# Optimization experiments

Hardware: AMD Instinct MI355X
Metric: run time of the kernel (lower is better)

Reference implementation:

```python
import jax, jax.numpy as jnp
import numpy as np

TEMP = 0.2
M, K, B = 8192, 128, 100


def setup_inputs() -> dict:
    key = jax.random.key(0)
    k1, k2, k3 = jax.random.split(key, 3)
    f = jax.random.normal(k1, (M, K), dtype=jnp.float32)
    features = f / jnp.linalg.norm(f, axis=1, keepdims=True)
    p = jax.random.normal(k2, (B, K), dtype=jnp.float32)
    protos = p / jnp.linalg.norm(p, axis=1, keepdims=True)
    labels = jax.random.randint(k3, (M,), 0, 2 * B, dtype=jnp.int32)
    proto_labels = jnp.arange(B, dtype=jnp.int32)
    return {"features": features, "labels": labels, "protos": protos, "proto_labels": proto_labels}


def reference(features, labels, protos, proto_labels):
    m = features.shape[0]
    dt = features.dtype
    # base = samples whose label appears among prototype labels
    base = (labels[None, :] == proto_labels[:, None]).any(axis=0)  # [M] bool
    novel = ~base
    nf = novel.astype(dt)
    bf = base.astype(dt)

    S = jnp.matmul(features, features.T) / TEMP          # [M, M] sample-sample logits
    P = jnp.matmul(features, protos.T) / TEMP            # [M, B] sample-proto logits

    # novel-novel pair mask: both novel, off-diagonal (fill_diagonal_(0))
    pair = nf[:, None] * nf[None, :] * (1.0 - jnp.eye(m, dtype=dt))  # [M, M]
    expS = jnp.exp(S)

    # --- novel loss (note: original adds RAW ni_pk.sum, not exp -- faithful) ---
    exp_sum = (expS * pair).sum(axis=1)                  # sum_{j novel, j!=i} exp(S_ij)
    denom = exp_sum + P.sum(axis=1)                      # + raw proto logit sum
    safe_den = jnp.where(novel, denom, 1.0)
    cnt = pair.sum(axis=1)                               # novel_label_mask is all-True 1D -> just pair count
    safe_cnt = jnp.where(cnt > 0, cnt, 1.0)
    # sum_j pair_ij * (S_ij - log(den_i)) = (S*pair).sum - log(den)*cnt
    num = (S * pair).sum(axis=1) - jnp.log(safe_den) * cnt
    loss_novel = (-(num / safe_cnt) * nf).sum()

    # --- base loss ---
    safe_lab = jnp.where(base, labels, 0)
    bi_pi = jnp.take_along_axis(P, safe_lab[:, None], axis=1)[:, 0]  # P[i, labels[i]]
    exp_nk = (expS * nf[None, :]).sum(axis=1)            # sum over novel columns
    exp_pk = jnp.exp(P).sum(axis=1)
    loss_base = (-(bi_pi - jnp.log(exp_nk + exp_pk)) * bf).sum()

    return (loss_novel + loss_base) / m
```

## Files before the change

### kernel.cpp

```cpp
#include <hip/hip_runtime.h>
#include <stdint.h>


#define M_TOT 8192
#define K_DIM 128
#define B_PRO 100
#define INV_T 5.0f
#define C_SCALE 7.2134752044448170f
#define INV_C   0.1386294361119891f
#define CJ    1024
#define NCHUNK (M_TOT / CJ)
#define PS    136
#define FS    136

#if __has_builtin(__builtin_amdgcn_exp2f)
#define EXP2(x) __builtin_amdgcn_exp2f(x)
#else
#define EXP2(x) __expf((x) * 0.6931471805599453f)
#endif

typedef __attribute__((ext_vector_type(8))) short  short8;
typedef __attribute__((ext_vector_type(4))) float  floatx4;

__device__ __forceinline__ float bf2f(unsigned short u) {
    union { unsigned int i; float f; } v; v.i = ((unsigned int)u) << 16; return v.f;
}
__device__ __forceinline__ unsigned short f2bf(float x) {
    union { float f; unsigned int i; } v; v.f = x;
    return (unsigned short)((v.i + 0x7fffu + ((v.i >> 16) & 1u)) >> 16);
}
__device__ __forceinline__ float lo_bf(unsigned int u) {
    union { unsigned int i; float f; } v; v.i = u << 16; return v.f;
}
__device__ __forceinline__ float hi_bf(unsigned int u) {
    union { unsigned int i; float f; } v; v.i = u & 0xffff0000u; return v.f;
}

__global__ __launch_bounds__(256) void k_proto2(
        const float* __restrict__ feat, const int* __restrict__ labels,
        const float* __restrict__ protos, const int* __restrict__ plabels,
        float* __restrict__ Psum, float* __restrict__ expPsum,
        float* __restrict__ PLab, int* __restrict__ nf,
        int* __restrict__ nfcnt,
        unsigned short* __restrict__ Fb, unsigned short* __restrict__ Fz,
        float* __restrict__ gpart, float* __restrict__ out) {
    __shared__ unsigned short protoB[128 * PS];
    __shared__ unsigned short featB[16 * FS];
    __shared__ float zcol[16][128];
    __shared__ int labL[16];
    __shared__ int plabL[B_PRO];
    __shared__ int novL[16];

    const int tid = threadIdx.x;
    const int rowBase = blockIdx.x * 16;

    if (blockIdx.x == 0 && tid == 0) out[0] = 0.f;

    if (tid < B_PRO) plabL[tid] = plabels[tid];
    if (tid >= 128 && tid < 144) labL[tid - 128] = labels[rowBase + tid - 128];

    {
        const int pr = tid >> 1, h = tid & 1;
        unsigned short* dst = &protoB[pr * PS + h * 64];
        if (pr < B_PRO) {
            const float* src = protos + pr * K_DIM + h * 64;
            #pragma unroll
            for (int j = 0; j < 16; ++j) {
                float4 v = ((const float4*)src)[j];
                *(ushort4*)&dst[j * 4] = make_ushort4(f2bf(v.x), f2bf(v.y), f2bf(v.z), f2bf(v.w));
            }
        } else {
            #pragma unroll
            for (int j = 0; j < 16; ++j) *(ushort4*)&dst[j * 4] = make_ushort4(0, 0, 0, 0);
        }
    }

    const int rp = tid >> 4, pq = tid & 15;
    float4 fa, fb4;
    {
        const float* src = feat + (size_t)(rowBase + rp) * K_DIM + pq * 8;
        fa  = ((const float4*)src)[0];
        fb4 = ((const float4*)src)[1];
        ushort4 o0 = make_ushort4(f2bf(fa.x), f2bf(fa.y), f2bf(fa.z), f2bf(fa.w));
        ushort4 o1 = make_ushort4(f2bf(fb4.x), f2bf(fb4.y), f2bf(fb4.z), f2bf(fb4.w));
        *(ushort4*)&featB[rp * FS + pq * 8]     = o0;
        *(ushort4*)&featB[rp * FS + pq * 8 + 4] = o1;
        unsigned short* fbd = Fb + (size_t)(rowBase + rp) * K_DIM + pq * 8;
        *(ushort4*)&fbd[0] = o0;
        *(ushort4*)&fbd[4] = o1;
    }
    __syncthreads();

    float acc[8];
    #pragma unroll
    for (int s = 0; s < 8; ++s) acc[s] = 0.f;

    const unsigned short* fRow = &featB[rp * FS];
    for (int kc = 0; kc < K_DIM; kc += 16) {
        uint4 q0 = *(const uint4*)&fRow[kc];
        uint4 q1 = *(const uint4*)&fRow[kc + 8];
        float f[16];
        f[0]=lo_bf(q0.x); f[1]=hi_bf(q0.x); f[2]=lo_bf(q0.y); f[3]=hi_bf(q0.y);
        f[4]=lo_bf(q0.z); f[5]=hi_bf(q0.z); f[6]=lo_bf(q0.w); f[7]=hi_bf(q0.w);
        f[8]=lo_bf(q1.x); f[9]=hi_bf(q1.x); f[10]=lo_bf(q1.y); f[11]=hi_bf(q1.y);
        f[12]=lo_bf(q1.z); f[13]=hi_bf(q1.z); f[14]=lo_bf(q1.w); f[15]=hi_bf(q1.w);
        #pragma unroll
        for (int s = 0; s < 8; ++s) {
            const int b = pq + (s & 3) * 16 + (s >> 2) * 64;
            const unsigned short* pRow = &protoB[b * PS];
            uint4 p0 = *(const uint4*)&pRow[kc];
            uint4 p1 = *(const uint4*)&pRow[kc + 8];
            float a = acc[s];
            a += lo_bf(p0.x)*f[0];  a += hi_bf(p0.x)*f[1];
            a += lo_bf(p0.y)*f[2];  a += hi_bf(p0.y)*f[3];
            a += lo_bf(p0.z)*f[4];  a += hi_bf(p0.z)*f[5];
            a += lo_bf(p0.w)*f[6];  a += hi_bf(p0.w)*f[7];
            a += lo_bf(p1.x)*f[8];  a += hi_bf(p1.x)*f[9];
            a += lo_bf(p1.y)*f[10]; a += hi_bf(p1.y)*f[11];
            a += lo_bf(p1.z)*f[12]; a += hi_bf(p1.z)*f[13];
            a += lo_bf(p1.w)*f[14]; a += hi_bf(p1.w)*f[15];
            acc[s] = a;
        }
    }

    const int lbl = labL[rp];
    float psum = 0.f, esum = 0.f, plab = 0.f, flg = 0.f;
    #pragma unroll
    for (int s = 0; s < 8; ++s) {
        const int b = pq + (s & 3) * 16 + (s >> 2) * 64;
        if (b < B_PRO) {
            const float Pv = acc[s] * INV_T;
            psum += Pv;
            esum += __expf(Pv);
            if (b == lbl) plab += Pv;
            if (plabL[b] == lbl) flg = 1.f;
        }
    }
    for (int off = 1; off < 16; off <<= 1) {
        psum += __shfl_xor(psum, off);
        esum += __shfl_xor(esum, off);
        plab += __shfl_xor(plab, off);
        flg  += __shfl_xor(flg,  off);
    }

    {
        const bool nov = (flg == 0.f);
        ushort4 z0 = make_ushort4(0,0,0,0), z1 = z0;
        if (nov) {
            z0 = make_ushort4(f2bf(fa.x*C_SCALE), f2bf(fa.y*C_SCALE),
                              f2bf(fa.z*C_SCALE), f2bf(fa.w*C_SCALE));
            z1 = make_ushort4(f2bf(fb4.x*C_SCALE), f2bf(fb4.y*C_SCALE),
                              f2bf(fb4.z*C_SCALE), f2bf(fb4.w*C_SCALE));
        }
        unsigned short* fzd = Fz + (size_t)(rowBase + rp) * K_DIM + pq * 8;
        *(ushort4*)&fzd[0] = z0;
        *(ushort4*)&fzd[4] = z1;
        float* zc = &zcol[rp][pq * 8];
        zc[0] = bf2f(z0.x); zc[1] = bf2f(z0.y); zc[2] = bf2f(z0.z); zc[3] = bf2f(z0.w);
        zc[4] = bf2f(z1.x); zc[5] = bf2f(z1.y); zc[6] = bf2f(z1.z); zc[7] = bf2f(z1.w);
    }

    if (pq == 0) {
        const int i = rowBase + rp;
        Psum[i] = psum; expPsum[i] = esum; PLab[i] = plab;
        const int nov = (flg > 0.f) ? 0 : 1;
        nf[i] = nov;
        novL[rp] = nov;
    }

    __syncthreads();
    if (tid < 128) {
        float s = 0.f;
        #pragma unroll
        for (int r = 0; r < 16; ++r) s += zcol[r][tid];
        gpart[blockIdx.x * 128 + tid] = s;
    } else if (tid == 255) {
        int c = 0;
        #pragma unroll
        for (int r = 0; r < 16; ++r) c += novL[r];
        nfcnt[blockIdx.x] = c;
    }
}

__global__ __launch_bounds__(256, 2) void k_main(const unsigned short* __restrict__ Fb,
                                                 const unsigned short* __restrict__ Fz,
                                                 float* __restrict__ rowSumPart,
                                                 const float* __restrict__ gpart,
                                                 const int* __restrict__ nfcnt,
                                                 float* __restrict__ gOut,
                                                 int* __restrict__ NnOut) {
    __shared__ float Re[4][64];
    __shared__ float gred[16][16];

    const int rowBase = blockIdx.y * 64;
    const int tid = threadIdx.x;
    const int wave = tid >> 6, lane = tid & 63;
    const int quad = lane >> 4, c = lane & 15;

    short8 a_frag[4][4];
    #pragma unroll
    for (int mt = 0; mt < 4; ++mt)
        #pragma unroll
        for (int ks = 0; ks < 4; ++ks)
            a_frag[mt][ks] = *(const short8*)(Fb + (size_t)(rowBase + mt * 16 + c) * K_DIM
                                              + ks * 32 + quad * 8);

    float accE[4][4];
    #pragma unroll
    for (int mt = 0; mt < 4; ++mt)
        #pragma unroll
        for (int r = 0; r < 4; ++r) accE[mt][r] = 0.f;

    const unsigned short* bptr = Fz + (size_t)(blockIdx.x * CJ + wave * 16 + c) * K_DIM
                                 + quad * 8;
    short8 c0 = *(const short8*)(bptr);
    short8 c1 = *(const short8*)(bptr + 32);
    short8 c2 = *(const short8*)(bptr + 64);
    short8 c3 = *(const short8*)(bptr + 96);

    const int NSTEP = CJ / 64;
    #pragma unroll 1
    for (int s = 0; s < NSTEP; ++s) {
        const unsigned short* np = bptr + ((s + 1 < NSTEP) ? (size_t)(64 * K_DIM) : 0);
        short8 n0 = *(const short8*)(np);
        short8 n1 = *(const short8*)(np + 32);
        short8 n2 = *(const short8*)(np + 64);
        short8 n3 = *(const short8*)(np + 96);
        bptr = np;

        floatx4 D[4];
        #pragma unroll
        for (int mt = 0; mt < 4; ++mt) D[mt] = (floatx4){0.f, 0.f, 0.f, 0.f};
        #pragma unroll
        for (int mt = 0; mt < 4; ++mt) {
            D[mt] = __builtin_amdgcn_mfma_f32_16x16x32_bf16(a_frag[mt][0], c0, D[mt], 0, 0, 0);
            D[mt] = __builtin_amdgcn_mfma_f32_16x16x32_bf16(a_frag[mt][1], c1, D[mt], 0, 0, 0);
            D[mt] = __builtin_amdgcn_mfma_f32_16x16x32_bf16(a_frag[mt][2], c2, D[mt], 0, 0, 0);
            D[mt] = __builtin_amdgcn_mfma_f32_16x16x32_bf16(a_frag[mt][3], c3, D[mt], 0, 0, 0);
        }
        #pragma unroll
        for (int mt = 0; mt < 4; ++mt)
            #pragma unroll
            for (int r = 0; r < 4; ++r)
                accE[mt][r] += EXP2(D[mt][r]);

        c0 = n0; c1 = n1; c2 = n2; c3 = n3;
    }

    #pragma unroll
    for (int mt = 0; mt < 4; ++mt)
        #pragma unroll
        for (int r = 0; r < 4; ++r) {
            float e = accE[mt][r];
            for (int off = 1; off < 16; off <<= 1) e += __shfl_xor(e, off);
            if (c == 0) Re[wave][mt * 16 + quad * 4 + r] = e;
        }
    __syncthreads();
    if (tid < 64) {
        const float e = Re[0][tid] + Re[1][tid] + Re[2][tid] + Re[3][tid];
        rowSumPart[(size_t)blockIdx.x * M_TOT + rowBase + tid] = e;
    }

    if (blockIdx.y == 0) {
        const int cl = (tid & 15) + 16 * blockIdx.x;
        const int rseg = tid >> 4;
        float s = 0.f;
        #pragma unroll 4
        for (int r = rseg; r < 512; r += 16) s += gpart[r * 128 + cl];
        gred[tid >> 4][tid & 15] = s;
        __syncthreads();
        if (tid < 16) {
            float t = 0.f;
            #pragma unroll
            for (int k = 0; k < 16; ++k) t += gred[k][tid];
            gOut[16 * blockIdx.x + tid] = t;
        }
        if (blockIdx.x == 0 && tid >= 64 && tid < 128) {
            const int l = tid - 64;
            int cs = 0;
            #pragma unroll
            for (int r = 0; r < 8; ++r) cs += nfcnt[l + 64 * r];
            for (int off = 1; off < 64; off <<= 1) cs += __shfl_xor(cs, off);
            if (l == 0) *NnOut = cs;
        }
    }
}

__global__ __launch_bounds__(256) void k_final(
        const int* __restrict__ nf,
        const float* __restrict__ rowSumPart,
        const float* __restrict__ Psum, const float* __restrict__ expPsum,
        const float* __restrict__ PLab,
        const unsigned short* __restrict__ Fb, const unsigned short* __restrict__ Fz,
        const float* __restrict__ gsrc, const int* __restrict__ NnPtr,
        float* __restrict__ out) {
    __shared__ float g[128];
    __shared__ float sh[16];
    __shared__ int shNn;
    const int tid = threadIdx.x;

    if (tid < 128) g[tid] = gsrc[tid];
    if (tid == 128) shNn = *NnPtr;
    __syncthreads();

    const int rp = tid >> 4, u = tid & 15;
    const int i = blockIdx.x * 16 + rp;
    uint4 qb = ((const uint4*)Fb)[(size_t)i * 16 + u];
    uint4 qz = ((const uint4*)Fz)[(size_t)i * 16 + u];
    float sZ = 0.f, dd = 0.f;
    {
        const float* gv = &g[u * 8];
        float fb[8], fz[8];
        fb[0]=lo_bf(qb.x); fb[1]=hi_bf(qb.x); fb[2]=lo_bf(qb.y); fb[3]=hi_bf(qb.y);
        fb[4]=lo_bf(qb.z); fb[5]=hi_bf(qb.z); fb[6]=lo_bf(qb.w); fb[7]=hi_bf(qb.w);
        fz[0]=lo_bf(qz.x); fz[1]=hi_bf(qz.x); fz[2]=lo_bf(qz.y); fz[3]=hi_bf(qz.y);
        fz[4]=lo_bf(qz.z); fz[5]=hi_bf(qz.z); fz[6]=lo_bf(qz.w); fz[7]=hi_bf(qz.w);
        #pragma unroll
        for (int e = 0; e < 8; ++e) { sZ += fb[e] * gv[e]; dd += fb[e] * fz[e]; }
    }
    float ep = (u < NCHUNK) ? rowSumPart[(size_t)u * M_TOT + i] : 0.f;
    for (int off = 1; off < 16; off <<= 1) {
        sZ += __shfl_xor(sZ, off);
        dd += __shfl_xor(dd, off);
        ep += __shfl_xor(ep, off);
    }

    if (u == 0) {
        const int Nn = shNn;
        const float nzero = (float)(M_TOT - Nn);
        const float sumEadj = ep - nzero;
        float contrib;
        if (nf[i]) {
            const float cnt = (float)(Nn - 1);
            const float sumE = sumEadj - EXP2(dd);
            const float denom = sumE + Psum[i];
            const float sumS_raw = (sZ - dd) * INV_C;
            const float num = INV_T * sumS_raw - logf(denom) * cnt;
            const float sc = cnt > 0.f ? cnt : 1.f;
            contrib = -(num / sc);
        } else {
            contrib = -(PLab[i] - logf(sumEadj + expPsum[i]));
        }
        sh[rp] = contrib;
    }
    __syncthreads();
    if (tid == 0) {
        float s = 0.f;
        #pragma unroll
        for (int r = 0; r < 16; ++r) s += sh[r];
        atomicAdd(out, s * (1.0f / (float)M_TOT));
    }
}

extern "C" void kernel_launch(void* const* d_in, const int* in_sizes, int n_in,
                              void* d_out, int out_size, void* d_ws, size_t ws_size,
                              hipStream_t stream) {
    const float* feat    = (const float*)d_in[0];
    const int*   labels  = (const int*)d_in[1];
    const float* protos  = (const float*)d_in[2];
    const int*   plabels = (const int*)d_in[3];
    float* out = (float*)d_out;

    char* ws = (char*)d_ws;
    int*   nfcnt      = (int*)ws;
    int*   NnOut      = (int*)(ws + 4096);
    float* gOut       = (float*)(ws + 4608);
    float* gpart      = (float*)(ws + 8192);
    float* rowSumPart = (float*)(ws + 270336);
    float* Psum       = (float*)(ws + 532480);
    float* expPsum    = (float*)(ws + 565248);
    float* PLab       = (float*)(ws + 598016);
    int*   nf         = (int*)(ws + 630784);
    unsigned short* Fb = (unsigned short*)(ws + 663552);
    unsigned short* Fz = (unsigned short*)(ws + 663552 + 2097152);

    k_proto2<<<M_TOT / 16, 256, 0, stream>>>(feat, labels, protos, plabels,
                                             Psum, expPsum, PLab, nf, nfcnt,
                                             Fb, Fz, gpart, out);
    dim3 gmain(NCHUNK, M_TOT / 64);
    k_main<<<gmain, 256, 0, stream>>>(Fb, Fz, rowSumPart, gpart, nfcnt, gOut, NnOut);
    k_final<<<M_TOT / 16, 256, 0, stream>>>(nf, rowSumPart, Psum, expPsum, PLab,
                                            Fb, Fz, gOut, NnOut, out);
}
```

Baseline: 124.2 us.

## Exploit symmetry of feature Gram matrix with triangular tile schedule

Replaces the full row-by-chunk exp-sum kernel with a kernel that computes only upper-triangular 128x128 tiles of the feature Gram matrix. Each tile contributes masked exp sums both to its rows and, via an LDS column reduction, to its columns, so the MFMA and exp work is roughly halved. Novel masking moves from zeroed scaled features to per-element multiplies by the novel flag, which removes the zero-column correction. The cost is extra per-element multiplies, a column-sum path with LDS writes, and a larger per-row partial buffer (64 slots) read in the final kernel.

```diff
diff --git a/kernel.cpp b/kernel.cpp
--- a/kernel.cpp
+++ b/kernel.cpp
@@ -8,8 +8,10 @@
 #define INV_T 5.0f
 #define C_SCALE 7.2134752044448170f
 #define INV_C   0.1386294361119891f
-#define CJ    1024
-#define NCHUNK (M_TOT / CJ)
+#define RT    128
+#define NT    (M_TOT / RT)
+#define NTILE (NT * (NT + 1) / 2)
+#define NSLOT NT
 #define PS    136
 #define FS    136
 
@@ -42,7 +44,7 @@
         float* __restrict__ Psum, float* __restrict__ expPsum,
         float* __restrict__ PLab, int* __restrict__ nf,
         int* __restrict__ nfcnt,
-        unsigned short* __restrict__ Fb, unsigned short* __restrict__ Fz,
+        unsigned short* __restrict__ Fb, unsigned short* __restrict__ Fc,
         float* __restrict__ gpart, float* __restrict__ out) {
     __shared__ unsigned short protoB[128 * PS];
     __shared__ unsigned short featB[16 * FS];
@@ -145,27 +147,25 @@
 
     {
         const bool nov = (flg == 0.f);
-        ushort4 z0 = make_ushort4(0,0,0,0), z1 = z0;
-        if (nov) {
-            z0 = make_ushort4(f2bf(fa.x*C_SCALE), f2bf(fa.y*C_SCALE),
-                              f2bf(fa.z*C_SCALE), f2bf(fa.w*C_SCALE));
-            z1 = make_ushort4(f2bf(fb4.x*C_SCALE), f2bf(fb4.y*C_SCALE),
-                              f2bf(fb4.z*C_SCALE), f2bf(fb4.w*C_SCALE));
-        }
-        unsigned short* fzd = Fz + (size_t)(rowBase + rp) * K_DIM + pq * 8;
-        *(ushort4*)&fzd[0] = z0;
-        *(ushort4*)&fzd[4] = z1;
+        ushort4 s0 = make_ushort4(f2bf(fa.x*C_SCALE), f2bf(fa.y*C_SCALE),
+                                  f2bf(fa.z*C_SCALE), f2bf(fa.w*C_SCALE));
+        ushort4 s1 = make_ushort4(f2bf(fb4.x*C_SCALE), f2bf(fb4.y*C_SCALE),
+                                  f2bf(fb4.z*C_SCALE), f2bf(fb4.w*C_SCALE));
+        unsigned short* fcd = Fc + (size_t)(rowBase + rp) * K_DIM + pq * 8;
+        *(ushort4*)&fcd[0] = s0;
+        *(ushort4*)&fcd[4] = s1;
+        const float m = nov ? 1.f : 0.f;
         float* zc = &zcol[rp][pq * 8];
-        zc[0] = bf2f(z0.x); zc[1] = bf2f(z0.y); zc[2] = bf2f(z0.z); zc[3] = bf2f(z0.w);
-        zc[4] = bf2f(z1.x); zc[5] = bf2f(z1.y); zc[6] = bf2f(z1.z); zc[7] = bf2f(z1.w);
-    }
-
-    if (pq == 0) {
-        const int i = rowBase + rp;
-        Psum[i] = psum; expPsum[i] = esum; PLab[i] = plab;
-        const int nov = (flg > 0.f) ? 0 : 1;
-        nf[i] = nov;
-        novL[rp] = nov;
+        zc[0] = m*bf2f(s0.x); zc[1] = m*bf2f(s0.y); zc[2] = m*bf2f(s0.z); zc[3] = m*bf2f(s0.w);
+        zc[4] = m*bf2f(s1.x); zc[5] = m*bf2f(s1.y); zc[6] = m*bf2f(s1.z); zc[7] = m*bf2f(s1.w);
+
+        if (pq == 0) {
+            const int i = rowBase + rp;
+            Psum[i] = psum; expPsum[i] = esum; PLab[i] = plab;
+            const int nv = nov ? 1 : 0;
+            nf[i] = nv;
+            novL[rp] = nv;
+        }
     }
 
     __syncthreads();
@@ -182,87 +182,119 @@
     }
 }
 
-__global__ __launch_bounds__(256, 2) void k_main(const unsigned short* __restrict__ Fb,
-                                                 const unsigned short* __restrict__ Fz,
-                                                 float* __restrict__ rowSumPart,
-                                                 const float* __restrict__ gpart,
-                                                 const int* __restrict__ nfcnt,
-                                                 float* __restrict__ gOut,
-                                                 int* __restrict__ NnOut) {
-    __shared__ float Re[4][64];
+__global__ __launch_bounds__(256, 2) void k_sym(
+        const unsigned short* __restrict__ Fb, const unsigned short* __restrict__ Fc,
+        const int* __restrict__ nf,
+        float* __restrict__ rowPart,
+        const float* __restrict__ gpart, const int* __restrict__ nfcnt,
+        float* __restrict__ gOut, int* __restrict__ NnOut) {
+    __shared__ float colLds[4][128];
     __shared__ float gred[16][16];
 
-    const int rowBase = blockIdx.y * 64;
+    const int t = blockIdx.x;
+    int a = (int)(((float)(2 * NT + 1)
+                   - sqrtf((float)((2 * NT + 1) * (2 * NT + 1) - 8 * t))) * 0.5f);
+    while ((a + 1) * NT - ((a + 1) * a) / 2 <= t) ++a;
+    while (a * NT - (a * (a - 1)) / 2 > t) --a;
+    const int b = a + (t - (a * NT - (a * (a - 1)) / 2));
+    const int R0 = a * RT, C0 = b * RT;
+
     const int tid = threadIdx.x;
     const int wave = tid >> 6, lane = tid & 63;
-    const int quad = lane >> 4, c = lane & 15;
-
-    short8 a_frag[4][4];
-    #pragma unroll
-    for (int mt = 0; mt < 4; ++mt)
+    const int quad = lane >> 4, cq = lane & 15;
+
+    short8 afr[2][4];
+    #pragma unroll
+    for (int mt = 0; mt < 2; ++mt)
         #pragma unroll
         for (int ks = 0; ks < 4; ++ks)
-            a_frag[mt][ks] = *(const short8*)(Fb + (size_t)(rowBase + mt * 16 + c) * K_DIM
-                                              + ks * 32 + quad * 8);
-
-    float accE[4][4];
-    #pragma unroll
-    for (int mt = 0; mt < 4; ++mt)
-        #pragma unroll
-        for (int r = 0; r < 4; ++r) accE[mt][r] = 0.f;
-
-    const unsigned short* bptr = Fz + (size_t)(blockIdx.x * CJ + wave * 16 + c) * K_DIM
-                                 + quad * 8;
-    short8 c0 = *(const short8*)(bptr);
-    short8 c1 = *(const short8*)(bptr + 32);
-    short8 c2 = *(const short8*)(bptr + 64);
-    short8 c3 = *(const short8*)(bptr + 96);
-
-    const int NSTEP = CJ / 64;
+            afr[mt][ks] = *(const short8*)(Fb
+                + (size_t)(R0 + wave * 32 + mt * 16 + cq) * K_DIM + ks * 32 + quad * 8);
+
+    float nmR[2][4];
+    #pragma unroll
+    for (int mt = 0; mt < 2; ++mt)
+        #pragma unroll
+        for (int r = 0; r < 4; ++r)
+            nmR[mt][r] = (float)nf[R0 + wave * 32 + mt * 16 + quad * 4 + r];
+
+    float accR[2][4];
+    #pragma unroll
+    for (int mt = 0; mt < 2; ++mt)
+        #pragma unroll
+        for (int r = 0; r < 4; ++r) accR[mt][r] = 0.f;
+
+    const unsigned short* bb = Fc + (size_t)(C0 + cq) * K_DIM + quad * 8;
+    short8 b0 = *(const short8*)(bb);
+    short8 b1 = *(const short8*)(bb + 32);
+    short8 b2 = *(const short8*)(bb + 64);
+    short8 b3 = *(const short8*)(bb + 96);
+    float nmc = (float)nf[C0 + cq];
+
     #pragma unroll 1
-    for (int s = 0; s < NSTEP; ++s) {
-        const unsigned short* np = bptr + ((s + 1 < NSTEP) ? (size_t)(64 * K_DIM) : 0);
-        short8 n0 = *(const short8*)(np);
-        short8 n1 = *(const short8*)(np + 32);
-        short8 n2 = *(const short8*)(np + 64);
-        short8 n3 = *(const short8*)(np + 96);
-        bptr = np;
-
-        floatx4 D[4];
-        #pragma unroll
-        for (int mt = 0; mt < 4; ++mt) D[mt] = (floatx4){0.f, 0.f, 0.f, 0.f};
-        #pragma unroll
-        for (int mt = 0; mt < 4; ++mt) {
-            D[mt] = __builtin_amdgcn_mfma_f32_16x16x32_bf16(a_frag[mt][0], c0, D[mt], 0, 0, 0);
-            D[mt] = __builtin_amdgcn_mfma_f32_16x16x32_bf16(a_frag[mt][1], c1, D[mt], 0, 0, 0);
-            D[mt] = __builtin_amdgcn_mfma_f32_16x16x32_bf16(a_frag[mt][2], c2, D[mt], 0, 0, 0);
-            D[mt] = __builtin_amdgcn_mfma_f32_16x16x32_bf16(a_frag[mt][3], c3, D[mt], 0, 0, 0);
-        }
-        #pragma unroll
-        for (int mt = 0; mt < 4; ++mt)
+    for (int ct = 0; ct < 8; ++ct) {
+        const int nx = (ct < 7) ? ct + 1 : ct;
+        const unsigned short* nb = Fc + (size_t)(C0 + nx * 16 + cq) * K_DIM + quad * 8;
+        short8 t0 = *(const short8*)(nb);
+        short8 t1 = *(const short8*)(nb + 32);
+        short8 t2 = *(const short8*)(nb + 64);
+        short8 t3 = *(const short8*)(nb + 96);
+        const float nmcn = (float)nf[C0 + nx * 16 + cq];
+
+        floatx4 D0 = (floatx4){0.f, 0.f, 0.f, 0.f};
+        floatx4 D1 = (floatx4){0.f, 0.f, 0.f, 0.f};
+        D0 = __builtin_amdgcn_mfma_f32_16x16x32_bf16(afr[0][0], b0, D0, 0, 0, 0);
+        D0 = __builtin_amdgcn_mfma_f32_16x16x32_bf16(afr[0][1], b1, D0, 0, 0, 0);
+        D0 = __builtin_amdgcn_mfma_f32_16x16x32_bf16(afr[0][2], b2, D0, 0, 0, 0);
+        D0 = __builtin_amdgcn_mfma_f32_16x16x32_bf16(afr[0][3], b3, D0, 0, 0, 0);
+        D1 = __builtin_amdgcn_mfma_f32_16x16x32_bf16(afr[1][0], b0, D1, 0, 0, 0);
+        D1 = __builtin_amdgcn_mfma_f32_16x16x32_bf16(afr[1][1], b1, D1, 0, 0, 0);
+        D1 = __builtin_amdgcn_mfma_f32_16x16x32_bf16(afr[1][2], b2, D1, 0, 0, 0);
+        D1 = __builtin_amdgcn_mfma_f32_16x16x32_bf16(afr[1][3], b3, D1, 0, 0, 0);
+
+        float cp = 0.f;
+        #pragma unroll
+        for (int r = 0; r < 4; ++r) {
+            const float e0 = EXP2(D0[r]);
+            accR[0][r] += e0 * nmc;
+            cp += e0 * nmR[0][r];
+            const float e1 = EXP2(D1[r]);
+            accR[1][r] += e1 * nmc;
+            cp += e1 * nmR[1][r];
+        }
+        cp += __shfl_xor(cp, 16);
+        cp += __shfl_xor(cp, 32);
+        if (quad == 0) colLds[wave][ct * 16 + cq] = cp;
+
+        b0 = t0; b1 = t1; b2 = t2; b3 = t3; nmc = nmcn;
+    }
+
+    #pragma unroll
+    for (int mt = 0; mt < 2; ++mt)
+        #pragma unroll
+        for (int r = 0; r < 4; ++r) {
+            float e = accR[mt][r];
+            e += __shfl_xor(e, 1); e += __shfl_xor(e, 2);
+            e += __shfl_xor(e, 4); e += __shfl_xor(e, 8);
+            accR[mt][r] = e;
+        }
+    if (cq == 0) {
+        #pragma unroll
+        for (int mt = 0; mt < 2; ++mt)
             #pragma unroll
             for (int r = 0; r < 4; ++r)
-                accE[mt][r] += EXP2(D[mt][r]);
-
-        c0 = n0; c1 = n1; c2 = n2; c3 = n3;
-    }
-
-    #pragma unroll
-    for (int mt = 0; mt < 4; ++mt)
-        #pragma unroll
-        for (int r = 0; r < 4; ++r) {
-            float e = accE[mt][r];
-            for (int off = 1; off < 16; off <<= 1) e += __shfl_xor(e, off);
-            if (c == 0) Re[wave][mt * 16 + quad * 4 + r] = e;
-        }
+                rowPart[(size_t)(R0 + wave * 32 + mt * 16 + quad * 4 + r) * NSLOT + b]
+                    = accR[mt][r];
+    }
+
     __syncthreads();
-    if (tid < 64) {
-        const float e = Re[0][tid] + Re[1][tid] + Re[2][tid] + Re[3][tid];
-        rowSumPart[(size_t)blockIdx.x * M_TOT + rowBase + tid] = e;
-    }
-
-    if (blockIdx.y == 0) {
-        const int cl = (tid & 15) + 16 * blockIdx.x;
+    if (tid < 128 && a != b) {
+        const float cs = colLds[0][tid] + colLds[1][tid] + colLds[2][tid] + colLds[3][tid];
+        rowPart[(size_t)(C0 + tid) * NSLOT + a] = cs;
+    }
+
+    if (a == b && a < 8) {
+        const int cl = (tid & 15) + 16 * a;
         const int rseg = tid >> 4;
         float s = 0.f;
         #pragma unroll 4
@@ -270,12 +302,12 @@
         gred[tid >> 4][tid & 15] = s;
         __syncthreads();
         if (tid < 16) {
-            float t = 0.f;
+            float tt = 0.f;
             #pragma unroll
-            for (int k = 0; k < 16; ++k) t += gred[k][tid];
-            gOut[16 * blockIdx.x + tid] = t;
-        }
-        if (blockIdx.x == 0 && tid >= 64 && tid < 128) {
+            for (int k = 0; k < 16; ++k) tt += gred[k][tid];
+            gOut[16 * a + tid] = tt;
+        }
+        if (a == 0 && tid >= 64 && tid < 128) {
             const int l = tid - 64;
             int cs = 0;
             #pragma unroll
@@ -288,10 +320,10 @@
 
 __global__ __launch_bounds__(256) void k_final(
         const int* __restrict__ nf,
-        const float* __restrict__ rowSumPart,
+        const float* __restrict__ rowPart,
         const float* __restrict__ Psum, const float* __restrict__ expPsum,
         const float* __restrict__ PLab,
-        const unsigned short* __restrict__ Fb, const unsigned short* __restrict__ Fz,
+        const unsigned short* __restrict__ Fb, const unsigned short* __restrict__ Fc,
         const float* __restrict__ gsrc, const int* __restrict__ NnPtr,
         float* __restrict__ out) {
     __shared__ float g[128];
@@ -306,7 +338,7 @@
     const int rp = tid >> 4, u = tid & 15;
     const int i = blockIdx.x * 16 + rp;
     uint4 qb = ((const uint4*)Fb)[(size_t)i * 16 + u];
-    uint4 qz = ((const uint4*)Fz)[(size_t)i * 16 + u];
+    uint4 qz = ((const uint4*)Fc)[(size_t)i * 16 + u];
     float sZ = 0.f, dd = 0.f;
     {
         const float* gv = &g[u * 8];
@@ -318,7 +350,8 @@
         #pragma unroll
         for (int e = 0; e < 8; ++e) { sZ += fb[e] * gv[e]; dd += fb[e] * fz[e]; }
     }
-    float ep = (u < NCHUNK) ? rowSumPart[(size_t)u * M_TOT + i] : 0.f;
+    float4 ev = ((const float4*)rowPart)[(size_t)i * 16 + u];
+    float ep = ev.x + ev.y + ev.z + ev.w;
     for (int off = 1; off < 16; off <<= 1) {
         sZ += __shfl_xor(sZ, off);
         dd += __shfl_xor(dd, off);
@@ -327,19 +360,17 @@
 
     if (u == 0) {
         const int Nn = shNn;
-        const float nzero = (float)(M_TOT - Nn);
-        const float sumEadj = ep - nzero;
         float contrib;
         if (nf[i]) {
             const float cnt = (float)(Nn - 1);
-            const float sumE = sumEadj - EXP2(dd);
+            const float sumE = ep - EXP2(dd);
             const float denom = sumE + Psum[i];
             const float sumS_raw = (sZ - dd) * INV_C;
             const float num = INV_T * sumS_raw - logf(denom) * cnt;
             const float sc = cnt > 0.f ? cnt : 1.f;
             contrib = -(num / sc);
         } else {
-            contrib = -(PLab[i] - logf(sumEadj + expPsum[i]));
+            contrib = -(PLab[i] - logf(ep + expPsum[i]));
         }
         sh[rp] = contrib;
     }
@@ -362,23 +393,22 @@
     float* out = (float*)d_out;
 
     char* ws = (char*)d_ws;
-    int*   nfcnt      = (int*)ws;
-    int*   NnOut      = (int*)(ws + 4096);
-    float* gOut       = (float*)(ws + 4608);
-    float* gpart      = (float*)(ws + 8192);
-    float* rowSumPart = (float*)(ws + 270336);
-    float* Psum       = (float*)(ws + 532480);
-    float* expPsum    = (float*)(ws + 565248);
-    float* PLab       = (float*)(ws + 598016);
-    int*   nf         = (int*)(ws + 630784);
-    unsigned short* Fb = (unsigned short*)(ws + 663552);
-    unsigned short* Fz = (unsigned short*)(ws + 663552 + 2097152);
+    int*   nfcnt   = (int*)ws;
+    int*   NnOut   = (int*)(ws + 4096);
+    float* gOut    = (float*)(ws + 4608);
+    float* gpart   = (float*)(ws + 8192);
+    float* rowPart = (float*)(ws + 270336);
+    float* Psum    = (float*)(ws + 2367488);
+    float* expPsum = (float*)(ws + 2400256);
+    float* PLab    = (float*)(ws + 2433024);
+    int*   nf      = (int*)(ws + 2465792);
+    unsigned short* Fb = (unsigned short*)(ws + 2498560);
+    unsigned short* Fc = (unsigned short*)(ws + 2498560 + 2097152);
 
     k_proto2<<<M_TOT / 16, 256, 0, stream>>>(feat, labels, protos, plabels,
                                              Psum, expPsum, PLab, nf, nfcnt,
-                                             Fb, Fz, gpart, out);
-    dim3 gmain(NCHUNK, M_TOT / 64);
-    k_main<<<gmain, 256, 0, stream>>>(Fb, Fz, rowSumPart, gpart, nfcnt, gOut, NnOut);
-    k_final<<<M_TOT / 16, 256, 0, stream>>>(nf, rowSumPart, Psum, expPsum, PLab,
-                                            Fb, Fz, gOut, NnOut, out);
-}
+                                             Fb, Fc, gpart, out);
+    k_sym<<<NTILE, 256, 0, stream>>>(Fb, Fc, nf, rowPart, gpart, nfcnt, gOut, NnOut);
+    k_final<<<M_TOT / 16, 256, 0, stream>>>(nf, rowPart, Psum, expPsum, PLab,
+                                            Fb, Fc, gOut, NnOut, out);
+}
```

New measurement: 132.8 us. 6.9% more time.
